# Kernel optimization log

Hardware: AMD Instinct MI355X
Metric: run time of the kernel (lower is better)

Reference implementation:

```python
import jax, jax.numpy as jnp
import numpy as np

B, S, N, D = 8, 2048, 512, 1024
MAX_W = 32  # fixed max span width (inclusive widths 0..MAX_W-1)
MASK_FILL = -1000.0


def setup_inputs() -> dict:
    key = jax.random.key(0)
    k1, k2, k3, k4 = jax.random.split(key, 4)
    sequence_tensor = jax.random.normal(k1, (B, S, D), dtype=jnp.float32)
    starts = jax.random.randint(k2, (B, N), 0, S - MAX_W)
    widths = jax.random.randint(k3, (B, N), 0, MAX_W)  # inclusive width = widths
    span_indices = jnp.stack([starts, starts + widths], axis=-1)  # (B, N, 2)
    att_w = jax.random.normal(k4, (D, 1), dtype=jnp.float32) * 0.02
    att_b = jnp.zeros((1,), dtype=jnp.float32)
    return {"sequence_tensor": sequence_tensor, "span_indices": span_indices,
            "att_w": att_w, "att_b": att_b}


def reference(sequence_tensor, span_indices, att_w, att_b):
    dtype = sequence_tensor.dtype
    starts = span_indices[..., 0]               # (B, N)
    ends = span_indices[..., 1]                 # (B, N), inclusive
    widths = ends - starts                      # (B, N)

    rng = jnp.arange(MAX_W)                     # (W,)
    raw_idx = ends[..., None] - rng             # (B, N, W), walks backward from end
    span_mask = (rng <= widths[..., None]) & (raw_idx >= 0)  # (B, N, W)
    idx = jnp.maximum(raw_idx, 0)               # relu on indices

    # global attention logits: (B, S, 1)
    logits = sequence_tensor @ att_w + att_b

    b, n = idx.shape[0], idx.shape[1]
    flat = idx.reshape(b, n * MAX_W)            # (B, N*W)
    # gather embeddings and logits over the time axis
    span_emb = jnp.take_along_axis(sequence_tensor, flat[..., None], axis=1)
    span_emb = span_emb.reshape(b, n, MAX_W, -1)              # (B, N, W, D)
    span_logits = jnp.take_along_axis(logits[..., 0], flat, axis=1)
    span_logits = span_logits.reshape(b, n, MAX_W)            # (B, N, W)

    # memory-efficient masked softmax: fill masked logits with -1000
    masked_logits = jnp.where(span_mask, span_logits, jnp.asarray(MASK_FILL, dtype))
    attn = jax.nn.softmax(masked_logits, axis=-1)             # (B, N, W)

    # weighted-sum pooling over span positions
    return jnp.einsum('bnw,bnwd->bnd', attn, span_emb)
```

## Files before the change

### kernel.cpp

```cpp
#include <hip/hip_runtime.h>
#include <hip/hip_bf16.h>

#define B 8
#define S 2048
#define N 512
#define D 1024
#define MAX_W 32
#define MASK_FILL -1000.0f
#define G 8
#define LOGITS_BLOCKS 2048

typedef float vfloat4 __attribute__((ext_vector_type(4)));

__global__ __launch_bounds__(512) void prep_kernel(
    const float* __restrict__ seq,
    const float* __restrict__ att_w,
    const float* __restrict__ att_b,
    const int*   __restrict__ spans,
    float* __restrict__ logits,
    int*   __restrict__ order)
{
    __shared__ unsigned short s_key[N];

    if (blockIdx.x < LOGITS_BLOCKS) {
        const int row  = blockIdx.x * 8 + (threadIdx.x >> 6);
        const int lane = threadIdx.x & 63;

        const float4* rp = (const float4*)(seq + (size_t)row * D);
        const float4* wp = (const float4*)att_w;

        float acc = 0.0f;
#pragma unroll
        for (int k = 0; k < 4; ++k) {
            const float4 a = rp[lane + 64 * k];
            const float4 w = wp[lane + 64 * k];
            acc += a.x * w.x + a.y * w.y + a.z * w.z + a.w * w.w;
        }
#pragma unroll
        for (int off = 32; off > 0; off >>= 1)
            acc += __shfl_down(acc, off);
        if (lane == 0)
            logits[row] = acc + att_b[0];
    } else {
        const int b = blockIdx.x - LOGITS_BLOCKS;
        const int n = threadIdx.x;

        const int key = spans[2 * (b * N + n) + 1];
        s_key[n] = (unsigned short)key;
        __syncthreads();

        int rank = 0;
#pragma unroll 8
        for (int j = 0; j < N; ++j) {
            const int kj = (int)s_key[j];
            rank += (kj < key) | ((kj == key) & (j < n));
        }
        order[b * N + rank] = n;
    }
}

__global__ __launch_bounds__(256) void pool_kernel(
    const float* __restrict__ seq,
    const int*   __restrict__ spans,
    const float* __restrict__ logits,
    const int*   __restrict__ order,
    float* __restrict__ out)
{
    const int b   = blockIdx.x & 7;
    const int grp = blockIdx.x >> 3;

    __shared__ int   s_n[G], s_st[G], s_en[G];
    __shared__ int   s_lohi[2];
    __shared__ float s_attn[G][MAX_W];

    const int tid = threadIdx.x;

    if (tid < G) {
        const int n = order[b * N + grp * G + tid];
        s_n[tid]  = n;
        s_st[tid] = spans[2 * (b * N + n) + 0];
        s_en[tid] = spans[2 * (b * N + n) + 1];
    }
    __syncthreads();

    if (tid == 0) {
        int lo = s_st[0], hi = s_en[0];
#pragma unroll
        for (int g = 1; g < G; ++g) {
            lo = min(lo, s_st[g]);
            hi = max(hi, s_en[g]);
        }
        s_lohi[0] = lo; s_lohi[1] = hi;
    }

    {
        const int g = tid >> 5, k = tid & 31;
        const int en  = s_en[g];
        const int wdt = en - s_st[g];
        const bool valid = (k <= wdt);
        const int  idx = max(en - k, 0);
        const float l = valid ? logits[b * S + idx] : MASK_FILL;

        float m = l;
#pragma unroll
        for (int off = 16; off > 0; off >>= 1)
            m = fmaxf(m, __shfl_down(m, off, 32));
        m = __shfl(m, 0, 32);

        const float p = __expf(l - m);

        float sum = p;
#pragma unroll
        for (int off = 16; off > 0; off >>= 1)
            sum += __shfl_down(sum, off, 32);
        sum = __shfl(sum, 0, 32);

        s_attn[g][k] = p / sum;
    }
    __syncthreads();

    const int lo = s_lohi[0], hi = s_lohi[1];

    int st[G], en[G];
#pragma unroll
    for (int g = 0; g < G; ++g) { st[g] = s_st[g]; en[g] = s_en[g]; }

    const float* sb = seq + (size_t)b * S * D;

    float4 acc[G];
#pragma unroll
    for (int g = 0; g < G; ++g) acc[g] = make_float4(0.f, 0.f, 0.f, 0.f);

    for (int s = lo; s <= hi; s += 4) {
        const int r1 = min(s + 1, hi);
        const int r2 = min(s + 2, hi);
        const int r3 = min(s + 3, hi);
        const float4 v0 = ((const float4*)(sb + (size_t)s  * D))[tid];
        const float4 v1 = ((const float4*)(sb + (size_t)r1 * D))[tid];
        const float4 v2 = ((const float4*)(sb + (size_t)r2 * D))[tid];
        const float4 v3 = ((const float4*)(sb + (size_t)r3 * D))[tid];

#pragma unroll
        for (int g = 0; g < G; ++g) {
            const int t = st[g], e = en[g];
            if (s <= e && s + 3 >= t) {
                const int o0 = e - s;
                const float a0 = (s     >= t && o0     >= 0) ? s_attn[g][o0 & 31]       : 0.f;
                const float a1 = (s + 1 >= t && o0 - 1 >= 0) ? s_attn[g][(o0 - 1) & 31] : 0.f;
                const float a2 = (s + 2 >= t && o0 - 2 >= 0) ? s_attn[g][(o0 - 2) & 31] : 0.f;
                const float a3 = (s + 3 >= t && o0 - 3 >= 0) ? s_attn[g][(o0 - 3) & 31] : 0.f;
                acc[g].x += a0 * v0.x + a1 * v1.x + a2 * v2.x + a3 * v3.x;
                acc[g].y += a0 * v0.y + a1 * v1.y + a2 * v2.y + a3 * v3.y;
                acc[g].z += a0 * v0.z + a1 * v1.z + a2 * v2.z + a3 * v3.z;
                acc[g].w += a0 * v0.w + a1 * v1.w + a2 * v2.w + a3 * v3.w;
            }
        }
    }

#pragma unroll
    for (int g = 0; g < G; ++g) {
        vfloat4 va;
        va.x = acc[g].x; va.y = acc[g].y; va.z = acc[g].z; va.w = acc[g].w;
        vfloat4* op = ((vfloat4*)(out + (size_t)(b * N + s_n[g]) * D)) + tid;
        __builtin_nontemporal_store(va, op);
    }
}

extern "C" void kernel_launch(void* const* d_in, const int* in_sizes, int n_in,
                              void* d_out, int out_size, void* d_ws, size_t ws_size,
                              hipStream_t stream)
{
    const float* seq    = (const float*)d_in[0];
    const int*   spans  = (const int*)  d_in[1];
    const float* att_w  = (const float*)d_in[2];
    const float* att_b  = (const float*)d_in[3];

    float* out    = (float*)d_out;
    float* logits = (float*)d_ws;
    int*   order  = (int*)((char*)d_ws + B * S * sizeof(float));

    prep_kernel<<<LOGITS_BLOCKS + B, 512, 0, stream>>>(seq, att_w, att_b,
                                                       spans, logits, order);
    pool_kernel<<<(B * N) / G, 256, 0, stream>>>(seq, spans, logits, order, out);
}
```

Baseline: 128.8 us.

## Split pool kernel across D chunks with scalar per-thread columns

```diff
diff --git a/kernel.cpp b/kernel.cpp
--- a/kernel.cpp
+++ b/kernel.cpp
@@ -8,6 +8,7 @@
 #define MAX_W 32
 #define MASK_FILL -1000.0f
 #define G 8
+#define DCH 4
 #define LOGITS_BLOCKS 2048
 
 typedef float vfloat4 __attribute__((ext_vector_type(4)));
@@ -66,14 +67,16 @@
     const int*   __restrict__ order,
     float* __restrict__ out)
 {
-    const int b   = blockIdx.x & 7;
-    const int grp = blockIdx.x >> 3;
+    const int b     = blockIdx.x & 7;
+    const int chunk = (blockIdx.x >> 3) & (DCH - 1);
+    const int grp   = blockIdx.x >> 5;
 
     __shared__ int   s_n[G], s_st[G], s_en[G];
     __shared__ int   s_lohi[2];
     __shared__ float s_attn[G][MAX_W];
 
     const int tid = threadIdx.x;
+    const int col = chunk * 256 + tid;
 
     if (tid < G) {
         const int n = order[b * N + grp * G + tid];
@@ -125,44 +128,38 @@
 #pragma unroll
     for (int g = 0; g < G; ++g) { st[g] = s_st[g]; en[g] = s_en[g]; }
 
-    const float* sb = seq + (size_t)b * S * D;
+    const float* sc = seq + (size_t)b * S * D + col;
 
-    float4 acc[G];
+    float acc[G];
 #pragma unroll
-    for (int g = 0; g < G; ++g) acc[g] = make_float4(0.f, 0.f, 0.f, 0.f);
+    for (int g = 0; g < G; ++g) acc[g] = 0.0f;
 
     for (int s = lo; s <= hi; s += 4) {
         const int r1 = min(s + 1, hi);
         const int r2 = min(s + 2, hi);
         const int r3 = min(s + 3, hi);
-        const float4 v0 = ((const float4*)(sb + (size_t)s  * D))[tid];
-        const float4 v1 = ((const float4*)(sb + (size_t)r1 * D))[tid];
-        const float4 v2 = ((const float4*)(sb + (size_t)r2 * D))[tid];
-        const float4 v3 = ((const float4*)(sb + (size_t)r3 * D))[tid];
+        const float v0 = sc[(size_t)s  * D];
+        const float v1 = sc[(size_t)r1 * D];
+        const float v2 = sc[(size_t)r2 * D];
+        const float v3 = sc[(size_t)r3 * D];
 
 #pragma unroll
         for (int g = 0; g < G; ++g) {
-            const int t = st[g], e = en[g];
-            if (s <= e && s + 3 >= t) {
-                const int o0 = e - s;
-                const float a0 = (s     >= t && o0     >= 0) ? s_attn[g][o0 & 31]       : 0.f;
-                const float a1 = (s + 1 >= t && o0 - 1 >= 0) ? s_attn[g][(o0 - 1) & 31] : 0.f;
-                const float a2 = (s + 2 >= t && o0 - 2 >= 0) ? s_attn[g][(o0 - 2) & 31] : 0.f;
-                const float a3 = (s + 3 >= t && o0 - 3 >= 0) ? s_attn[g][(o0 - 3) & 31] : 0.f;
-                acc[g].x += a0 * v0.x + a1 * v1.x + a2 * v2.x + a3 * v3.x;
-                acc[g].y += a0 * v0.y + a1 * v1.y + a2 * v2.y + a3 * v3.y;
-                acc[g].z += a0 * v0.z + a1 * v1.z + a2 * v2.z + a3 * v3.z;
-                acc[g].w += a0 * v0.w + a1 * v1.w + a2 * v2.w + a3 * v3.w;
+            if (s <= en[g] && s + 3 >= st[g]) {
+                const int o0 = en[g] - s;
+                const float a0 = ((unsigned)o0       < 32u) ? s_attn[g][o0]     : 0.f;
+                const float a1 = ((unsigned)(o0 - 1) < 32u) ? s_attn[g][o0 - 1] : 0.f;
+                const float a2 = ((unsigned)(o0 - 2) < 32u) ? s_attn[g][o0 - 2] : 0.f;
+                const float a3 = ((unsigned)(o0 - 3) < 32u) ? s_attn[g][o0 - 3] : 0.f;
+                acc[g] += a0 * v0 + a1 * v1 + a2 * v2 + a3 * v3;
             }
         }
     }
 
 #pragma unroll
     for (int g = 0; g < G; ++g) {
-        vfloat4 va;
-        va.x = acc[g].x; va.y = acc[g].y; va.z = acc[g].z; va.w = acc[g].w;
-        vfloat4* op = ((vfloat4*)(out + (size_t)(b * N + s_n[g]) * D)) + tid;
-        __builtin_nontemporal_store(va, op);
+        float* op = out + (size_t)(b * N + s_n[g]) * D + col;
+        __builtin_nontemporal_store(acc[g], op);
     }
 }
 
@@ -181,5 +178,6 @@
 
     prep_kernel<<<LOGITS_BLOCKS + B, 512, 0, stream>>>(seq, att_w, att_b,
                                                        spans, logits, order);
-    pool_kernel<<<(B * N) / G, 256, 0, stream>>>(seq, spans, logits, order, out);
+    pool_kernel<<<(B * N / G) * DCH, 256, 0, stream>>>(seq, spans, logits,
+                                                       order, out);
 }
```

Result: slower. 135.8 us (+5.4%).

## Stage bf16 copy of sequence in prep and pool two spans per block

Applied to the files above, without the earlier changes.

```diff
diff --git a/kernel.cpp b/kernel.cpp
--- a/kernel.cpp
+++ b/kernel.cpp
@@ -7,10 +7,16 @@
 #define D 1024
 #define MAX_W 32
 #define MASK_FILL -1000.0f
-#define G 8
-#define LOGITS_BLOCKS 2048
+#define G 2
+#define PREP_BLOCKS 2048
 
 typedef float vfloat4 __attribute__((ext_vector_type(4)));
+
+__device__ inline unsigned short f2bf(float f) {
+    unsigned u = __float_as_uint(f);
+    u += 0x7fff + ((u >> 16) & 1);
+    return (unsigned short)(u >> 16);
+}
 
 __global__ __launch_bounds__(512) void prep_kernel(
     const float* __restrict__ seq,
@@ -18,31 +24,43 @@
     const float* __restrict__ att_b,
     const int*   __restrict__ spans,
     float* __restrict__ logits,
-    int*   __restrict__ order)
+    unsigned short* __restrict__ seqh,
+    int* __restrict__ order)
 {
     __shared__ unsigned short s_key[N];
 
-    if (blockIdx.x < LOGITS_BLOCKS) {
+    if (blockIdx.x < PREP_BLOCKS) {
         const int row  = blockIdx.x * 8 + (threadIdx.x >> 6);
         const int lane = threadIdx.x & 63;
 
         const float4* rp = (const float4*)(seq + (size_t)row * D);
         const float4* wp = (const float4*)att_w;
 
+        float4 a[4];
         float acc = 0.0f;
 #pragma unroll
         for (int k = 0; k < 4; ++k) {
-            const float4 a = rp[lane + 64 * k];
+            a[k] = rp[lane + 64 * k];
             const float4 w = wp[lane + 64 * k];
-            acc += a.x * w.x + a.y * w.y + a.z * w.z + a.w * w.w;
+            acc += a[k].x * w.x + a[k].y * w.y + a[k].z * w.z + a[k].w * w.w;
         }
+
+        ushort4* hp = (ushort4*)(seqh + (size_t)row * D);
+#pragma unroll
+        for (int k = 0; k < 4; ++k) {
+            ushort4 h;
+            h.x = f2bf(a[k].x); h.y = f2bf(a[k].y);
+            h.z = f2bf(a[k].z); h.w = f2bf(a[k].w);
+            hp[lane + 64 * k] = h;
+        }
+
 #pragma unroll
         for (int off = 32; off > 0; off >>= 1)
             acc += __shfl_down(acc, off);
         if (lane == 0)
             logits[row] = acc + att_b[0];
     } else {
-        const int b = blockIdx.x - LOGITS_BLOCKS;
+        const int b = blockIdx.x - PREP_BLOCKS;
         const int n = threadIdx.x;
 
         const int key = spans[2 * (b * N + n) + 1];
@@ -60,7 +78,7 @@
 }
 
 __global__ __launch_bounds__(256) void pool_kernel(
-    const float* __restrict__ seq,
+    const unsigned short* __restrict__ seqh,
     const int*   __restrict__ spans,
     const float* __restrict__ logits,
     const int*   __restrict__ order,
@@ -70,7 +88,6 @@
     const int grp = blockIdx.x >> 3;
 
     __shared__ int   s_n[G], s_st[G], s_en[G];
-    __shared__ int   s_lohi[2];
     __shared__ float s_attn[G][MAX_W];
 
     const int tid = threadIdx.x;
@@ -83,17 +100,7 @@
     }
     __syncthreads();
 
-    if (tid == 0) {
-        int lo = s_st[0], hi = s_en[0];
-#pragma unroll
-        for (int g = 1; g < G; ++g) {
-            lo = min(lo, s_st[g]);
-            hi = max(hi, s_en[g]);
-        }
-        s_lohi[0] = lo; s_lohi[1] = hi;
-    }
-
-    {
+    if (tid < 64) {
         const int g = tid >> 5, k = tid & 31;
         const int en  = s_en[g];
         const int wdt = en - s_st[g];
@@ -119,49 +126,61 @@
     }
     __syncthreads();
 
-    const int lo = s_lohi[0], hi = s_lohi[1];
-
-    int st[G], en[G];
-#pragma unroll
-    for (int g = 0; g < G; ++g) { st[g] = s_st[g]; en[g] = s_en[g]; }
-
-    const float* sb = seq + (size_t)b * S * D;
-
-    float4 acc[G];
-#pragma unroll
-    for (int g = 0; g < G; ++g) acc[g] = make_float4(0.f, 0.f, 0.f, 0.f);
+    const int st0 = s_st[0], en0 = s_en[0];
+    const int st1 = s_st[1], en1 = s_en[1];
+    const int lo = min(st0, st1);
+    const int hi = max(en0, en1);
+
+    const unsigned short* sb = seqh + (size_t)b * S * D;
+
+    float4 acc0 = make_float4(0.f, 0.f, 0.f, 0.f);
+    float4 acc1 = make_float4(0.f, 0.f, 0.f, 0.f);
 
     for (int s = lo; s <= hi; s += 4) {
         const int r1 = min(s + 1, hi);
         const int r2 = min(s + 2, hi);
         const int r3 = min(s + 3, hi);
-        const float4 v0 = ((const float4*)(sb + (size_t)s  * D))[tid];
-        const float4 v1 = ((const float4*)(sb + (size_t)r1 * D))[tid];
-        const float4 v2 = ((const float4*)(sb + (size_t)r2 * D))[tid];
-        const float4 v3 = ((const float4*)(sb + (size_t)r3 * D))[tid];
-
-#pragma unroll
-        for (int g = 0; g < G; ++g) {
-            const int t = st[g], e = en[g];
-            if (s <= e && s + 3 >= t) {
-                const int o0 = e - s;
-                const float a0 = (s     >= t && o0     >= 0) ? s_attn[g][o0 & 31]       : 0.f;
-                const float a1 = (s + 1 >= t && o0 - 1 >= 0) ? s_attn[g][(o0 - 1) & 31] : 0.f;
-                const float a2 = (s + 2 >= t && o0 - 2 >= 0) ? s_attn[g][(o0 - 2) & 31] : 0.f;
-                const float a3 = (s + 3 >= t && o0 - 3 >= 0) ? s_attn[g][(o0 - 3) & 31] : 0.f;
-                acc[g].x += a0 * v0.x + a1 * v1.x + a2 * v2.x + a3 * v3.x;
-                acc[g].y += a0 * v0.y + a1 * v1.y + a2 * v2.y + a3 * v3.y;
-                acc[g].z += a0 * v0.z + a1 * v1.z + a2 * v2.z + a3 * v3.z;
-                acc[g].w += a0 * v0.w + a1 * v1.w + a2 * v2.w + a3 * v3.w;
-            }
-        }
-    }
-
-#pragma unroll
-    for (int g = 0; g < G; ++g) {
+        const uint2 q0 = ((const uint2*)(sb + (size_t)s  * D))[tid];
+        const uint2 q1 = ((const uint2*)(sb + (size_t)r1 * D))[tid];
+        const uint2 q2 = ((const uint2*)(sb + (size_t)r2 * D))[tid];
+        const uint2 q3 = ((const uint2*)(sb + (size_t)r3 * D))[tid];
+
+        const int o0 = en0 - s;
+        const int p0 = en1 - s;
+        const float a00 = ((unsigned)o0       < 32u) ? s_attn[0][o0]     : 0.f;
+        const float a01 = ((unsigned)(o0 - 1) < 32u) ? s_attn[0][o0 - 1] : 0.f;
+        const float a02 = ((unsigned)(o0 - 2) < 32u) ? s_attn[0][o0 - 2] : 0.f;
+        const float a03 = ((unsigned)(o0 - 3) < 32u) ? s_attn[0][o0 - 3] : 0.f;
+        const float a10 = ((unsigned)p0       < 32u) ? s_attn[1][p0]     : 0.f;
+        const float a11 = ((unsigned)(p0 - 1) < 32u) ? s_attn[1][p0 - 1] : 0.f;
+        const float a12 = ((unsigned)(p0 - 2) < 32u) ? s_attn[1][p0 - 2] : 0.f;
+        const float a13 = ((unsigned)(p0 - 3) < 32u) ? s_attn[1][p0 - 3] : 0.f;
+
+#define BL(u) __uint_as_float((u) << 16)
+#define BH(u) __uint_as_float((u) & 0xffff0000u)
+        const float vx0 = BL(q0.x), vy0 = BH(q0.x), vz0 = BL(q0.y), vw0 = BH(q0.y);
+        const float vx1 = BL(q1.x), vy1 = BH(q1.x), vz1 = BL(q1.y), vw1 = BH(q1.y);
+        const float vx2 = BL(q2.x), vy2 = BH(q2.x), vz2 = BL(q2.y), vw2 = BH(q2.y);
+        const float vx3 = BL(q3.x), vy3 = BH(q3.x), vz3 = BL(q3.y), vw3 = BH(q3.y);
+#undef BL
+#undef BH
+        acc0.x += a00 * vx0 + a01 * vx1 + a02 * vx2 + a03 * vx3;
+        acc0.y += a00 * vy0 + a01 * vy1 + a02 * vy2 + a03 * vy3;
+        acc0.z += a00 * vz0 + a01 * vz1 + a02 * vz2 + a03 * vz3;
+        acc0.w += a00 * vw0 + a01 * vw1 + a02 * vw2 + a03 * vw3;
+        acc1.x += a10 * vx0 + a11 * vx1 + a12 * vx2 + a13 * vx3;
+        acc1.y += a10 * vy0 + a11 * vy1 + a12 * vy2 + a13 * vy3;
+        acc1.z += a10 * vz0 + a11 * vz1 + a12 * vz2 + a13 * vz3;
+        acc1.w += a10 * vw0 + a11 * vw1 + a12 * vw2 + a13 * vw3;
+    }
+
+    {
         vfloat4 va;
-        va.x = acc[g].x; va.y = acc[g].y; va.z = acc[g].z; va.w = acc[g].w;
-        vfloat4* op = ((vfloat4*)(out + (size_t)(b * N + s_n[g]) * D)) + tid;
+        va.x = acc0.x; va.y = acc0.y; va.z = acc0.z; va.w = acc0.w;
+        vfloat4* op = ((vfloat4*)(out + (size_t)(b * N + s_n[0]) * D)) + tid;
+        __builtin_nontemporal_store(va, op);
+        va.x = acc1.x; va.y = acc1.y; va.z = acc1.z; va.w = acc1.w;
+        op = ((vfloat4*)(out + (size_t)(b * N + s_n[1]) * D)) + tid;
         __builtin_nontemporal_store(va, op);
     }
 }
@@ -177,9 +196,13 @@
 
     float* out    = (float*)d_out;
     float* logits = (float*)d_ws;
-    int*   order  = (int*)((char*)d_ws + B * S * sizeof(float));
-
-    prep_kernel<<<LOGITS_BLOCKS + B, 512, 0, stream>>>(seq, att_w, att_b,
-                                                       spans, logits, order);
-    pool_kernel<<<(B * N) / G, 256, 0, stream>>>(seq, spans, logits, order, out);
-}
+    unsigned short* seqh =
+        (unsigned short*)((char*)d_ws + (size_t)B * S * sizeof(float));
+    int* order =
+        (int*)((char*)d_ws + (size_t)B * S * sizeof(float)
+                           + (size_t)B * S * D * sizeof(unsigned short));
+
+    prep_kernel<<<PREP_BLOCKS + B, 512, 0, stream>>>(seq, att_w, att_b, spans,
+                                                     logits, seqh, order);
+    pool_kernel<<<(B * N) / G, 256, 0, stream>>>(seqh, spans, logits, order, out);
+}
```

New measurement: 128.8 us. No clear change (-0.0%).
